# Performance work log

Hardware: AMD Instinct MI355X
Metric: run time of the kernel (lower is better)

The kernel has to match this reference:

```python
import jax, jax.numpy as jnp
import numpy as np

D_MODEL = 1024
NUM_HEADS = 16
HEAD_DIM = D_MODEL // NUM_HEADS
B, S = 4, 2048


def setup_inputs() -> dict:
    key = jax.random.key(0)
    ks = jax.random.split(key, 12)
    s = 1.0 / np.sqrt(D_MODEL)
    return {
        "inputs_q": jax.random.normal(ks[0], (B, S, D_MODEL), jnp.float32),
        "inputs_k": jax.random.normal(ks[1], (B, S, D_MODEL), jnp.float32),
        "inputs_v": jax.random.normal(ks[2], (B, S, D_MODEL), jnp.float32),
        "Wq": jax.random.normal(ks[3], (D_MODEL, D_MODEL), jnp.float32) * s,
        "bq": jax.random.normal(ks[4], (D_MODEL,), jnp.float32) * 0.01,
        "Wk": jax.random.normal(ks[5], (D_MODEL, D_MODEL), jnp.float32) * s,
        "bk": jax.random.normal(ks[6], (D_MODEL,), jnp.float32) * 0.01,
        "Wv": jax.random.normal(ks[7], (D_MODEL, D_MODEL), jnp.float32) * s,
        "bv": jax.random.normal(ks[8], (D_MODEL,), jnp.float32) * 0.01,
        "Wo": jax.random.normal(ks[9], (D_MODEL, D_MODEL), jnp.float32) * s,
        "bo": jax.random.normal(ks[10], (D_MODEL,), jnp.float32) * 0.01,
    }


def reference(inputs_q, inputs_k, inputs_v, Wq, bq, Wk, bk, Wv, bv, Wo, bo):
    b, s, _ = inputs_q.shape
    # linear projections
    q = inputs_q @ Wq + bq  # [b, s, d_model]
    k = inputs_k @ Wk + bk
    v = inputs_v @ Wv + bv
    # split heads: bsd -> bhsd
    q = q.reshape(b, s, NUM_HEADS, HEAD_DIM).transpose(0, 2, 1, 3)
    k = k.reshape(b, s, NUM_HEADS, HEAD_DIM).transpose(0, 2, 1, 3)
    v = v.reshape(b, s, NUM_HEADS, HEAD_DIM).transpose(0, 2, 1, 3)
    scale = 1.0 / jnp.sqrt(jnp.asarray(HEAD_DIM, q.dtype))
    scores = jnp.einsum('bhqd,bhkd->bhqk', q, k) * scale  # [b,h,s,s]
    # causal mask: position q attends to k <= q
    causal = jnp.tril(jnp.ones((s, s), dtype=bool))
    scores = jnp.where(causal[None, None], scores, jnp.asarray(-jnp.inf, scores.dtype))
    attn = jax.nn.softmax(scores, axis=-1)
    ctx = jnp.einsum('bhqk,bhkd->bhqd', attn, v)  # [b,h,s,hd]
    ctx = ctx.transpose(0, 2, 1, 3).reshape(b, s, D_MODEL)
    return ctx @ Wo + bo
```

## Files before the change

### kernel.cpp

```cpp
#include <hip/hip_runtime.h>
#include <math.h>
#include <type_traits>

typedef __bf16 bf16;
typedef __attribute__((ext_vector_type(8))) __bf16 bf16x8;
typedef __attribute__((ext_vector_type(4))) float f32x4;
typedef __attribute__((ext_vector_type(16))) float f32x16;

#define SEQ 2048
#define DM 1024
#define NH 16
#define HD 64
#define BATCH 4

#define NEG_BIG (-1e30f)
#define SCALE_L2E 0.18033688011f

__device__ inline bf16x8 pack_bf16x8(f32x4 x0, f32x4 x1) {
  bf16x8 r;
  r[0] = (bf16)x0[0]; r[1] = (bf16)x0[1]; r[2] = (bf16)x0[2]; r[3] = (bf16)x0[3];
  r[4] = (bf16)x1[0]; r[5] = (bf16)x1[1]; r[6] = (bf16)x1[2]; r[7] = (bf16)x1[3];
  return r;
}

__device__ inline void async_copy16(const bf16* g, bf16* l) {
  __builtin_amdgcn_global_load_lds(
      (const __attribute__((address_space(1))) unsigned int*)g,
      (__attribute__((address_space(3))) unsigned int*)l, 16, 0, 0);
}

__global__ __launch_bounds__(256) void transpose_w_kernel(
    const float* __restrict__ Wq, const float* __restrict__ Wk,
    const float* __restrict__ Wv, const float* __restrict__ Wo,
    bf16* __restrict__ Tq, bf16* __restrict__ Tk,
    bf16* __restrict__ Tv, bf16* __restrict__ To) {
  __shared__ bf16 tile[64 * 66];
  int z = blockIdx.z;
  const float* src = (z == 0) ? Wq : (z == 1) ? Wk : (z == 2) ? Wv : Wo;
  bf16* dst = (z == 0) ? Tq : (z == 1) ? Tk : (z == 2) ? Tv : To;
  int n0 = blockIdx.x * 64, k0 = blockIdx.y * 64;
  int t = threadIdx.x;
  int c = t & 63, rr = t >> 6;
#pragma unroll
  for (int i = 0; i < 16; i++) {
    int k = i * 4 + rr;
    tile[k * 66 + c] = (bf16)src[(size_t)(k0 + k) * DM + n0 + c];
  }
  __syncthreads();
#pragma unroll
  for (int i = 0; i < 16; i++) {
    int n = i * 4 + rr;
    dst[(size_t)(n0 + n) * DM + k0 + c] = tile[c * 66 + n];
  }
}

__global__ __launch_bounds__(256) void qkv_gemm_kernel(
    const float* __restrict__ Aq, const float* __restrict__ Ak,
    const float* __restrict__ Av, const bf16* __restrict__ Tq,
    const bf16* __restrict__ Tk, const bf16* __restrict__ Tv,
    const float* __restrict__ bq, const float* __restrict__ bk,
    const float* __restrict__ bv, bf16* __restrict__ Cq,
    bf16* __restrict__ Ck, bf16* __restrict__ Cv) {
  int z = blockIdx.z;
  const float* A = (z == 0) ? Aq : (z == 1) ? Ak : Av;
  const bf16* Bt = (z == 0) ? Tq : (z == 1) ? Tk : Tv;
  const float* bias = (z == 0) ? bq : (z == 1) ? bk : bv;
  bf16* C = (z == 0) ? Cq : (z == 1) ? Ck : Cv;

  __shared__ bf16 As[2][128 * 32];
  __shared__ bf16 Bs[2][128 * 32];
  int m0 = blockIdx.x * 128, n0 = blockIdx.y * 128;
  int t = threadIdx.x;
  int wave = t >> 6, lane = t & 63, lr = lane & 15, lq = lane >> 4;
  int wm = (wave & 1) * 64, wn = (wave >> 1) * 64;

  f32x4 acc[4][4];
#pragma unroll
  for (int i = 0; i < 4; i++)
#pragma unroll
    for (int j = 0; j < 4; j++) acc[i][j] = (f32x4){0.f, 0.f, 0.f, 0.f};

  int arow = t >> 2;
  int acolf = (t & 3) * 8;
  const float* gA = A + (size_t)(m0 + arow) * DM + acolf;
  const float* gA2 = gA + (size_t)64 * DM;
  f32x4 ar[2][2];

  auto loadA = [&](int k0) {
    ar[0][0] = *(const f32x4*)(gA + k0);
    ar[0][1] = *(const f32x4*)(gA + k0 + 4);
    ar[1][0] = *(const f32x4*)(gA2 + k0);
    ar[1][1] = *(const f32x4*)(gA2 + k0 + 4);
  };
  auto cvtwriteA = [&](int buf) {
    *(bf16x8*)&As[buf][arow * 32 + acolf] = pack_bf16x8(ar[0][0], ar[0][1]);
    *(bf16x8*)&As[buf][(arow + 64) * 32 + acolf] =
        pack_bf16x8(ar[1][0], ar[1][1]);
  };

  int srow = wave * 32 + (lane >> 2);
  int skc = lane & 3;
  const bf16* gB0 = Bt + (size_t)(n0 + srow) * DM + skc * 8;
  const bf16* gB1 = gB0 + (size_t)16 * DM;
  int oB0 = (wave * 128) * 8;
  int oB1 = (wave * 128 + 64) * 8;
  auto stageB = [&](int buf) {
    async_copy16(gB0, &Bs[buf][oB0]);
    async_copy16(gB1, &Bs[buf][oB1]);
    gB0 += 32; gB1 += 32;
  };

  loadA(0);
  stageB(0);
  cvtwriteA(0);
  __syncthreads();

  int cur = 0;
  for (int k0 = 0; k0 < DM; k0 += 32) {
    bool more = (k0 + 32 < DM);
    if (more) {
      loadA(k0 + 32);
      stageB(cur ^ 1);
    }

    bf16x8 af[4], bfr[4];
#pragma unroll
    for (int i = 0; i < 4; i++)
      af[i] = *(const bf16x8*)&As[cur][(wm + i * 16 + lr) * 32 + lq * 8];
#pragma unroll
    for (int j = 0; j < 4; j++)
      bfr[j] = *(const bf16x8*)&Bs[cur][(wn + j * 16 + lr) * 32 + lq * 8];
    __builtin_amdgcn_s_setprio(1);
#pragma unroll
    for (int i = 0; i < 4; i++)
#pragma unroll
      for (int j = 0; j < 4; j++)
        acc[i][j] = __builtin_amdgcn_mfma_f32_16x16x32_bf16(af[i], bfr[j],
                                                            acc[i][j], 0, 0, 0);
    __builtin_amdgcn_s_setprio(0);
    if (more) cvtwriteA(cur ^ 1);
    __syncthreads();
    cur ^= 1;
  }

#pragma unroll
  for (int j = 0; j < 4; j++) {
    int col = n0 + wn + j * 16 + lr;
    float bv2 = bias[col];
#pragma unroll
    for (int i = 0; i < 4; i++) {
      int row0 = m0 + wm + i * 16 + lq * 4;
#pragma unroll
      for (int r = 0; r < 4; r++) {
        int row = row0 + r;
        float v = acc[i][j][r] + bv2;
        int b = row >> 11, s = row & 2047, h = col >> 6, d = col & 63;
        if (z < 2) {
          C[((size_t)(b * NH + h) * SEQ + s) * HD + d] = (bf16)v;
        } else {
          C[((size_t)(b * NH + h) * HD + d) * SEQ + s] = (bf16)v;
        }
      }
    }
  }
}

template <typename CT, int MODE>
__global__ __launch_bounds__(256) void gemm_bias_kernel(
    const bf16* __restrict__ A, const bf16* __restrict__ Bt,
    const float* __restrict__ bias, CT* __restrict__ C) {
  __shared__ bf16 As[2][128 * 32];
  __shared__ bf16 Bs[2][128 * 32];
  int m0 = blockIdx.x * 128, n0 = blockIdx.y * 128;
  int t = threadIdx.x;
  int wave = t >> 6, lane = t & 63, lr = lane & 15, lq = lane >> 4;
  int wm = (wave & 1) * 64, wn = (wave >> 1) * 64;

  f32x4 acc[4][4];
#pragma unroll
  for (int i = 0; i < 4; i++)
#pragma unroll
    for (int j = 0; j < 4; j++) acc[i][j] = (f32x4){0.f, 0.f, 0.f, 0.f};

  int srow = wave * 32 + (lane >> 2);
  int skc = lane & 3;
  const bf16* gA0 = A + (size_t)(m0 + srow) * DM + skc * 8;
  const bf16* gA1 = gA0 + (size_t)16 * DM;
  const bf16* gB0 = Bt + (size_t)(n0 + srow) * DM + skc * 8;
  const bf16* gB1 = gB0 + (size_t)16 * DM;
  int oA0 = (wave * 128) * 8;
  int oA1 = (wave * 128 + 64) * 8;

  auto stage = [&](int buf) {
    async_copy16(gA0, &As[buf][oA0]);
    async_copy16(gA1, &As[buf][oA1]);
    async_copy16(gB0, &Bs[buf][oA0]);
    async_copy16(gB1, &Bs[buf][oA1]);
    gA0 += 32; gA1 += 32; gB0 += 32; gB1 += 32;
  };

  stage(0);
  __syncthreads();
  int cur = 0;
  for (int k0 = 0; k0 < DM; k0 += 32) {
    if (k0 + 32 < DM) stage(cur ^ 1);

    bf16x8 af[4], bfr[4];
#pragma unroll
    for (int i = 0; i < 4; i++)
      af[i] = *(const bf16x8*)&As[cur][(wm + i * 16 + lr) * 32 + lq * 8];
#pragma unroll
    for (int j = 0; j < 4; j++)
      bfr[j] = *(const bf16x8*)&Bs[cur][(wn + j * 16 + lr) * 32 + lq * 8];
    __builtin_amdgcn_s_setprio(1);
#pragma unroll
    for (int i = 0; i < 4; i++)
#pragma unroll
      for (int j = 0; j < 4; j++)
        acc[i][j] = __builtin_amdgcn_mfma_f32_16x16x32_bf16(af[i], bfr[j],
                                                            acc[i][j], 0, 0, 0);
    __builtin_amdgcn_s_setprio(0);
    __syncthreads();
    cur ^= 1;
  }

#pragma unroll
  for (int j = 0; j < 4; j++) {
    int col = n0 + wn + j * 16 + lr;
    float bv = bias[col];
#pragma unroll
    for (int i = 0; i < 4; i++) {
      int row0 = m0 + wm + i * 16 + lq * 4;
#pragma unroll
      for (int r = 0; r < 4; r++) {
        int row = row0 + r;
        float v = acc[i][j][r] + bv;
        if constexpr (MODE == 0) {
          C[(size_t)row * DM + col] = (CT)v;
        } else {
          int b = row >> 11, s = row & 2047, h = col >> 6, d = col & 63;
          C[((size_t)(b * NH + h) * SEQ + s) * HD + d] = (CT)v;
        }
      }
    }
  }
}

__global__ __launch_bounds__(256, 2) void attention_kernel(
    const bf16* __restrict__ Qc, const bf16* __restrict__ Kc,
    const bf16* __restrict__ Vt, bf16* __restrict__ ctx) {
  int t = threadIdx.x, wave = t >> 6, lane = t & 63;
  int l31 = lane & 31, hh = lane >> 5;

  int bid = blockIdx.x;
  int xcd = bid & 7, qq = bid >> 3;
  int g = xcd + 8 * (qq & 7);
  int bx = qq >> 3;
  int h = g & 15, b = g >> 4;
  int p = bx * 4 + wave;

  const bf16* Qb = Qc + (size_t)(b * NH + h) * SEQ * HD;
  const bf16* Kb = Kc + (size_t)(b * NH + h) * SEQ * HD;
  const bf16* Vb = Vt + (size_t)(b * NH + h) * HD * SEQ;
  bf16* Cb = ctx + (size_t)b * SEQ * DM + h * HD;

#pragma unroll 1
  for (int pass = 0; pass < 2; pass++) {
    int tq = pass ? (63 - p) : p;
    int q0 = tq * 32;

    bf16x8 qf[4];
#pragma unroll
    for (int st = 0; st < 4; st++)
      qf[st] = *(const bf16x8*)&Qb[(size_t)(q0 + l31) * HD + st * 16 + hh * 8];

    f32x16 o[2];
#pragma unroll
    for (int dt = 0; dt < 2; dt++)
#pragma unroll
      for (int r = 0; r < 16; r++) o[dt][r] = 0.f;
    float m_st = NEG_BIG, l_st = 0.f;

    int nch = (tq >> 1) + 1;
#pragma unroll 1
    for (int c = 0; c < nch; c++) {
      int kv0 = c * 64;
      bf16x8 kf[2][4];
#pragma unroll
      for (int kt = 0; kt < 2; kt++)
#pragma unroll
        for (int st = 0; st < 4; st++)
          kf[kt][st] = *(const bf16x8*)&Kb[(size_t)(kv0 + kt * 32 + l31) * HD +
                                           st * 16 + hh * 8];
      bf16x8 vf[2][4];
#pragma unroll
      for (int dt = 0; dt < 2; dt++)
#pragma unroll
        for (int ks = 0; ks < 4; ks++)
          vf[dt][ks] = *(const bf16x8*)&Vb[(size_t)(dt * 32 + l31) * SEQ + kv0 +
                                           ks * 16 + hh * 8];

      f32x16 s[2];
      __builtin_amdgcn_s_setprio(1);
#pragma unroll
      for (int kt = 0; kt < 2; kt++) {
        f32x16 acc;
#pragma unroll
        for (int r = 0; r < 16; r++) acc[r] = 0.f;
#pragma unroll
        for (int st = 0; st < 4; st++)
          acc = __builtin_amdgcn_mfma_f32_32x32x16_bf16(kf[kt][st], qf[st],
                                                        acc, 0, 0, 0);
        s[kt] = acc;
      }
      __builtin_amdgcn_s_setprio(0);

      bool diag = (c == nch - 1);
      if (diag) {
        int q_g = q0 + l31;
#pragma unroll
        for (int kt = 0; kt < 2; kt++)
#pragma unroll
          for (int r = 0; r < 16; r++) {
            int key = kv0 + kt * 32 + (r & 3) + 8 * (r >> 2) + 4 * hh;
            float v = s[kt][r] * SCALE_L2E;
            s[kt][r] = (key > q_g) ? NEG_BIG : v;
          }
      } else {
#pragma unroll
        for (int kt = 0; kt < 2; kt++)
#pragma unroll
          for (int r = 0; r < 16; r++) s[kt][r] *= SCALE_L2E;
      }

      float mx = s[0][0];
#pragma unroll
      for (int r = 1; r < 16; r++) mx = fmaxf(mx, s[0][r]);
#pragma unroll
      for (int r = 0; r < 16; r++) mx = fmaxf(mx, s[1][r]);
      mx = fmaxf(mx, __shfl_xor(mx, 32));
      float mnew = fmaxf(m_st, mx);
      float alpha = exp2f(m_st - mnew);
      m_st = mnew;
      float rs = 0.f;
#pragma unroll
      for (int kt = 0; kt < 2; kt++)
#pragma unroll
        for (int r = 0; r < 16; r++) {
          float pv = exp2f(s[kt][r] - mnew);
          s[kt][r] = pv;
          rs += pv;
        }
      rs += __shfl_xor(rs, 32);
      l_st = l_st * alpha + rs;
#pragma unroll
      for (int dt = 0; dt < 2; dt++)
#pragma unroll
        for (int r = 0; r < 16; r++) o[dt][r] *= alpha;

      unsigned int W[2][8];
#pragma unroll
      for (int kt = 0; kt < 2; kt++)
#pragma unroll
        for (int w = 0; w < 8; w++) {
          unsigned int u;
          asm("v_cvt_pk_bf16_f32 %0, %1, %2"
              : "=v"(u)
              : "v"(s[kt][2 * w]), "v"(s[kt][2 * w + 1]));
          W[kt][w] = u;
        }
      bf16x8 pf[4];
#pragma unroll
      for (int kt = 0; kt < 2; kt++) {
        unsigned int x1 = hh ? W[kt][0] : W[kt][2];
        unsigned int x2 = hh ? W[kt][1] : W[kt][3];
        unsigned int x3 = hh ? W[kt][4] : W[kt][6];
        unsigned int x4 = hh ? W[kt][5] : W[kt][7];
        unsigned int y1 = (unsigned int)__shfl_xor((int)x1, 32);
        unsigned int y2 = (unsigned int)__shfl_xor((int)x2, 32);
        unsigned int y3 = (unsigned int)__shfl_xor((int)x3, 32);
        unsigned int y4 = (unsigned int)__shfl_xor((int)x4, 32);
        unsigned int* f0 = (unsigned int*)&pf[2 * kt];
        unsigned int* f1 = (unsigned int*)&pf[2 * kt + 1];
        f0[0] = hh ? y1 : W[kt][0];
        f0[1] = hh ? y2 : W[kt][1];
        f0[2] = hh ? W[kt][2] : y1;
        f0[3] = hh ? W[kt][3] : y2;
        f1[0] = hh ? y3 : W[kt][4];
        f1[1] = hh ? y4 : W[kt][5];
        f1[2] = hh ? W[kt][6] : y3;
        f1[3] = hh ? W[kt][7] : y4;
      }

      __builtin_amdgcn_s_setprio(1);
#pragma unroll
      for (int dt = 0; dt < 2; dt++)
#pragma unroll
        for (int ks = 0; ks < 4; ks++)
          o[dt] = __builtin_amdgcn_mfma_f32_32x32x16_bf16(vf[dt][ks], pf[ks],
                                                          o[dt], 0, 0, 0);
      __builtin_amdgcn_s_setprio(0);
    }

    float inv = 1.f / l_st;
    int row = q0 + l31;
#pragma unroll
    for (int dt = 0; dt < 2; dt++)
#pragma unroll
      for (int r = 0; r < 16; r += 2) {
        float va = o[dt][r] * inv;
        float vb = o[dt][r + 1] * inv;
        unsigned int u;
        asm("v_cvt_pk_bf16_f32 %0, %1, %2" : "=v"(u) : "v"(va), "v"(vb));
        int d = dt * 32 + (r & 3) + 8 * (r >> 2) + 4 * hh;
        *(unsigned int*)&Cb[(size_t)row * DM + d] = u;
      }
  }
}

extern "C" void kernel_launch(void* const* d_in, const int* in_sizes, int n_in,
                              void* d_out, int out_size, void* d_ws,
                              size_t ws_size, hipStream_t stream) {
  const float* iq = (const float*)d_in[0];
  const float* ik = (const float*)d_in[1];
  const float* iv = (const float*)d_in[2];
  const float* Wq = (const float*)d_in[3];
  const float* bq = (const float*)d_in[4];
  const float* Wk = (const float*)d_in[5];
  const float* bk = (const float*)d_in[6];
  const float* Wv = (const float*)d_in[7];
  const float* bv = (const float*)d_in[8];
  const float* Wo = (const float*)d_in[9];
  const float* bo = (const float*)d_in[10];

  char* ws = (char*)d_ws;
  const size_t MB = 1024 * 1024;
  bf16* Tq = (bf16*)(ws + 0 * MB);
  bf16* Tk = (bf16*)(ws + 2 * MB);
  bf16* Tv = (bf16*)(ws + 4 * MB);
  bf16* To = (bf16*)(ws + 6 * MB);
  bf16* Qc = (bf16*)(ws + 8 * MB);
  bf16* Kc = (bf16*)(ws + 24 * MB);
  bf16* Cx = (bf16*)(ws + 40 * MB);
  bf16* Vtp = (bf16*)d_out;

  transpose_w_kernel<<<dim3(16, 16, 4), 256, 0, stream>>>(Wq, Wk, Wv, Wo, Tq,
                                                          Tk, Tv, To);
  qkv_gemm_kernel<<<dim3(64, 8, 3), 256, 0, stream>>>(
      iq, ik, iv, Tq, Tk, Tv, bq, bk, bv, Qc, Kc, Vtp);
  attention_kernel<<<dim3(512), 256, 0, stream>>>(Qc, Kc, Vtp, Cx);
  gemm_bias_kernel<float, 0><<<dim3(64, 8), 256, 0, stream>>>(Cx, To, bo,
                                                              (float*)d_out);
}
```

Baseline: 405.4 us.

## Split attention KV range across four waves with LDS softmax merge

Each block now handles one 32-row query tile per pass, and its four waves split that tile's causal KV range in 32-key chunks. Partial outputs, maxima and sums are merged in LDS by wave 0 using a flash-decoding style combine. The grid grows from 512 to 2048 blocks and launch bounds go up to 4 blocks per SM, so there are more waves in flight and the causal work is spread more evenly. The cost is two block barriers per tile, an LDS round trip of partial results, a serial merge done by one wave, and smaller 32-key chunks that give less MFMA work per softmax step.

Result: slower. 423.5 us (+4.5%).

```diff
diff --git a/kernel.cpp b/kernel.cpp
--- a/kernel.cpp
+++ b/kernel.cpp
@@ -246,9 +246,12 @@
   }
 }
 
-__global__ __launch_bounds__(256, 2) void attention_kernel(
+__global__ __launch_bounds__(256, 4) void attention_kernel(
     const bf16* __restrict__ Qc, const bf16* __restrict__ Kc,
     const bf16* __restrict__ Vt, bf16* __restrict__ ctx) {
+  __shared__ float ls_o[3][2][16][64];
+  __shared__ float ls_ml[3][2][64];
+
   int t = threadIdx.x, wave = t >> 6, lane = t & 63;
   int l31 = lane & 31, hh = lane >> 5;
 
@@ -257,7 +260,6 @@
   int g = xcd + 8 * (qq & 7);
   int bx = qq >> 3;
   int h = g & 15, b = g >> 4;
-  int p = bx * 4 + wave;
 
   const bf16* Qb = Qc + (size_t)(b * NH + h) * SEQ * HD;
   const bf16* Kb = Kc + (size_t)(b * NH + h) * SEQ * HD;
@@ -265,9 +267,12 @@
   bf16* Cb = ctx + (size_t)b * SEQ * DM + h * HD;
 
 #pragma unroll 1
-  for (int pass = 0; pass < 2; pass++) {
-    int tq = pass ? (63 - p) : p;
+  for (int ti = 0; ti < 2; ti++) {
+    int tq = ti ? (63 - bx) : bx;
     int q0 = tq * 32;
+    int nch = tq + 1;
+    int c0 = (nch * wave) >> 2;
+    int c1 = (nch * (wave + 1)) >> 2;
 
     bf16x8 qf[4];
 #pragma unroll
@@ -281,76 +286,58 @@
       for (int r = 0; r < 16; r++) o[dt][r] = 0.f;
     float m_st = NEG_BIG, l_st = 0.f;
 
-    int nch = (tq >> 1) + 1;
 #pragma unroll 1
-    for (int c = 0; c < nch; c++) {
-      int kv0 = c * 64;
-      bf16x8 kf[2][4];
-#pragma unroll
-      for (int kt = 0; kt < 2; kt++)
-#pragma unroll
-        for (int st = 0; st < 4; st++)
-          kf[kt][st] = *(const bf16x8*)&Kb[(size_t)(kv0 + kt * 32 + l31) * HD +
-                                           st * 16 + hh * 8];
-      bf16x8 vf[2][4];
+    for (int c = c0; c < c1; c++) {
+      int kv0 = c * 32;
+      bf16x8 kf[4];
+#pragma unroll
+      for (int st = 0; st < 4; st++)
+        kf[st] =
+            *(const bf16x8*)&Kb[(size_t)(kv0 + l31) * HD + st * 16 + hh * 8];
+      bf16x8 vf[2][2];
 #pragma unroll
       for (int dt = 0; dt < 2; dt++)
 #pragma unroll
-        for (int ks = 0; ks < 4; ks++)
+        for (int ks = 0; ks < 2; ks++)
           vf[dt][ks] = *(const bf16x8*)&Vb[(size_t)(dt * 32 + l31) * SEQ + kv0 +
                                            ks * 16 + hh * 8];
 
-      f32x16 s[2];
+      f32x16 s;
+#pragma unroll
+      for (int r = 0; r < 16; r++) s[r] = 0.f;
       __builtin_amdgcn_s_setprio(1);
 #pragma unroll
-      for (int kt = 0; kt < 2; kt++) {
-        f32x16 acc;
-#pragma unroll
-        for (int r = 0; r < 16; r++) acc[r] = 0.f;
-#pragma unroll
-        for (int st = 0; st < 4; st++)
-          acc = __builtin_amdgcn_mfma_f32_32x32x16_bf16(kf[kt][st], qf[st],
-                                                        acc, 0, 0, 0);
-        s[kt] = acc;
-      }
+      for (int st = 0; st < 4; st++)
+        s = __builtin_amdgcn_mfma_f32_32x32x16_bf16(kf[st], qf[st], s, 0, 0, 0);
       __builtin_amdgcn_s_setprio(0);
 
-      bool diag = (c == nch - 1);
-      if (diag) {
+      if (c == nch - 1) {
         int q_g = q0 + l31;
 #pragma unroll
-        for (int kt = 0; kt < 2; kt++)
-#pragma unroll
-          for (int r = 0; r < 16; r++) {
-            int key = kv0 + kt * 32 + (r & 3) + 8 * (r >> 2) + 4 * hh;
-            float v = s[kt][r] * SCALE_L2E;
-            s[kt][r] = (key > q_g) ? NEG_BIG : v;
-          }
+        for (int r = 0; r < 16; r++) {
+          int key = kv0 + (r & 3) + 8 * (r >> 2) + 4 * hh;
+          float v = s[r] * SCALE_L2E;
+          s[r] = (key > q_g) ? NEG_BIG : v;
+        }
       } else {
 #pragma unroll
-        for (int kt = 0; kt < 2; kt++)
-#pragma unroll
-          for (int r = 0; r < 16; r++) s[kt][r] *= SCALE_L2E;
-      }
-
-      float mx = s[0][0];
-#pragma unroll
-      for (int r = 1; r < 16; r++) mx = fmaxf(mx, s[0][r]);
-#pragma unroll
-      for (int r = 0; r < 16; r++) mx = fmaxf(mx, s[1][r]);
+        for (int r = 0; r < 16; r++) s[r] *= SCALE_L2E;
+      }
+
+      float mx = s[0];
+#pragma unroll
+      for (int r = 1; r < 16; r++) mx = fmaxf(mx, s[r]);
       mx = fmaxf(mx, __shfl_xor(mx, 32));
       float mnew = fmaxf(m_st, mx);
       float alpha = exp2f(m_st - mnew);
       m_st = mnew;
       float rs = 0.f;
 #pragma unroll
-      for (int kt = 0; kt < 2; kt++)
-#pragma unroll
-        for (int r = 0; r < 16; r++) {
-          float pv = exp2f(s[kt][r] - mnew);
-          s[kt][r] = pv;
-          rs += pv;
-        }
+      for (int r = 0; r < 16; r++) {
+        float pv = exp2f(s[r] - mnew);
+        s[r] = pv;
+        rs += pv;
+      }
       rs += __shfl_xor(rs, 32);
       l_st = l_st * alpha + rs;
 #pragma unroll
@@ -358,63 +345,93 @@
 #pragma unroll
         for (int r = 0; r < 16; r++) o[dt][r] *= alpha;
 
-      unsigned int W[2][8];
-#pragma unroll
-      for (int kt = 0; kt < 2; kt++)
-#pragma unroll
-        for (int w = 0; w < 8; w++) {
-          unsigned int u;
-          asm("v_cvt_pk_bf16_f32 %0, %1, %2"
-              : "=v"(u)
-              : "v"(s[kt][2 * w]), "v"(s[kt][2 * w + 1]));
-          W[kt][w] = u;
-        }
-      bf16x8 pf[4];
-#pragma unroll
-      for (int kt = 0; kt < 2; kt++) {
-        unsigned int x1 = hh ? W[kt][0] : W[kt][2];
-        unsigned int x2 = hh ? W[kt][1] : W[kt][3];
-        unsigned int x3 = hh ? W[kt][4] : W[kt][6];
-        unsigned int x4 = hh ? W[kt][5] : W[kt][7];
+      unsigned int W[8];
+#pragma unroll
+      for (int w = 0; w < 8; w++) {
+        unsigned int u;
+        asm("v_cvt_pk_bf16_f32 %0, %1, %2"
+            : "=v"(u)
+            : "v"(s[2 * w]), "v"(s[2 * w + 1]));
+        W[w] = u;
+      }
+      bf16x8 pf[2];
+      {
+        unsigned int x1 = hh ? W[0] : W[2];
+        unsigned int x2 = hh ? W[1] : W[3];
+        unsigned int x3 = hh ? W[4] : W[6];
+        unsigned int x4 = hh ? W[5] : W[7];
         unsigned int y1 = (unsigned int)__shfl_xor((int)x1, 32);
         unsigned int y2 = (unsigned int)__shfl_xor((int)x2, 32);
         unsigned int y3 = (unsigned int)__shfl_xor((int)x3, 32);
         unsigned int y4 = (unsigned int)__shfl_xor((int)x4, 32);
-        unsigned int* f0 = (unsigned int*)&pf[2 * kt];
-        unsigned int* f1 = (unsigned int*)&pf[2 * kt + 1];
-        f0[0] = hh ? y1 : W[kt][0];
-        f0[1] = hh ? y2 : W[kt][1];
-        f0[2] = hh ? W[kt][2] : y1;
-        f0[3] = hh ? W[kt][3] : y2;
-        f1[0] = hh ? y3 : W[kt][4];
-        f1[1] = hh ? y4 : W[kt][5];
-        f1[2] = hh ? W[kt][6] : y3;
-        f1[3] = hh ? W[kt][7] : y4;
+        unsigned int* f0 = (unsigned int*)&pf[0];
+        unsigned int* f1 = (unsigned int*)&pf[1];
+        f0[0] = hh ? y1 : W[0];
+        f0[1] = hh ? y2 : W[1];
+        f0[2] = hh ? W[2] : y1;
+        f0[3] = hh ? W[3] : y2;
+        f1[0] = hh ? y3 : W[4];
+        f1[1] = hh ? y4 : W[5];
+        f1[2] = hh ? W[6] : y3;
+        f1[3] = hh ? W[7] : y4;
       }
 
       __builtin_amdgcn_s_setprio(1);
 #pragma unroll
       for (int dt = 0; dt < 2; dt++)
 #pragma unroll
-        for (int ks = 0; ks < 4; ks++)
+        for (int ks = 0; ks < 2; ks++)
           o[dt] = __builtin_amdgcn_mfma_f32_32x32x16_bf16(vf[dt][ks], pf[ks],
                                                           o[dt], 0, 0, 0);
       __builtin_amdgcn_s_setprio(0);
     }
 
-    float inv = 1.f / l_st;
-    int row = q0 + l31;
-#pragma unroll
-    for (int dt = 0; dt < 2; dt++)
-#pragma unroll
-      for (int r = 0; r < 16; r += 2) {
-        float va = o[dt][r] * inv;
-        float vb = o[dt][r + 1] * inv;
-        unsigned int u;
-        asm("v_cvt_pk_bf16_f32 %0, %1, %2" : "=v"(u) : "v"(va), "v"(vb));
-        int d = dt * 32 + (r & 3) + 8 * (r >> 2) + 4 * hh;
-        *(unsigned int*)&Cb[(size_t)row * DM + d] = u;
-      }
+    if (wave != 0) {
+#pragma unroll
+      for (int dt = 0; dt < 2; dt++)
+#pragma unroll
+        for (int r = 0; r < 16; r++) ls_o[wave - 1][dt][r][lane] = o[dt][r];
+      ls_ml[wave - 1][0][lane] = m_st;
+      ls_ml[wave - 1][1][lane] = l_st;
+    }
+    __syncthreads();
+    if (wave == 0) {
+      float M = m_st;
+      float mw[3];
+#pragma unroll
+      for (int w = 0; w < 3; w++) {
+        mw[w] = ls_ml[w][0][lane];
+        M = fmaxf(M, mw[w]);
+      }
+      float a0 = exp2f(m_st - M);
+      float aw[3];
+#pragma unroll
+      for (int w = 0; w < 3; w++) aw[w] = exp2f(mw[w] - M);
+      float L = l_st * a0;
+#pragma unroll
+      for (int w = 0; w < 3; w++) L += ls_ml[w][1][lane] * aw[w];
+      float linv = 1.f / L;
+      int row = q0 + l31;
+#pragma unroll
+      for (int dt = 0; dt < 2; dt++)
+#pragma unroll
+        for (int r = 0; r < 16; r += 2) {
+          float va = o[dt][r] * a0;
+          float vb = o[dt][r + 1] * a0;
+#pragma unroll
+          for (int w = 0; w < 3; w++) {
+            va += ls_o[w][dt][r][lane] * aw[w];
+            vb += ls_o[w][dt][r + 1][lane] * aw[w];
+          }
+          va *= linv;
+          vb *= linv;
+          unsigned int u;
+          asm("v_cvt_pk_bf16_f32 %0, %1, %2" : "=v"(u) : "v"(va), "v"(vb));
+          int d = dt * 32 + (r & 3) + 8 * (r >> 2) + 4 * hh;
+          *(unsigned int*)&Cb[(size_t)row * DM + d] = u;
+        }
+    }
+    __syncthreads();
   }
 }
 
@@ -448,7 +465,7 @@
                                                           Tk, Tv, To);
   qkv_gemm_kernel<<<dim3(64, 8, 3), 256, 0, stream>>>(
       iq, ik, iv, Tq, Tk, Tv, bq, bk, bv, Qc, Kc, Vtp);
-  attention_kernel<<<dim3(512), 256, 0, stream>>>(Qc, Kc, Vtp, Cx);
+  attention_kernel<<<dim3(2048), 256, 0, stream>>>(Qc, Kc, Vtp, Cx);
   gemm_bias_kernel<float, 0><<<dim3(64, 8), 256, 0, stream>>>(Cx, To, bo,
                                                               (float*)d_out);
 }
```
